# Kernel optimization log

Hardware: AMD Instinct MI355X
Metric: run time of the kernel (lower is better)

Reference implementation:

```python
import math
import jax, jax.numpy as jnp
import numpy as np

B, L, DIM = 8, 8192, 512
H = 8
DH = DIM // H
KS = 13          # kernel_size
DIL = 2          # dilation


def na1d_indices(length, kernel_size, dilation):
    """NATTEN 1D window-start and positional-bias-start indices, vectorized."""
    ns = kernel_size // 2  # neighborhood radius
    i = jnp.arange(length)
    if dilation <= 1:
        ws = jnp.maximum(i - ns, 0) + jnp.where(i + ns >= length, length - i - ns - 1, 0)
        ps = ns + jnp.where(i < ns, ns - i, 0) + jnp.where(i + ns >= length, length - i - 1 - ns, 0)
    else:
        imodd = i % dilation
        a = (length // dilation) * dilation
        b = length - a
        hi = jnp.where(imodd < b,
                       length - b + imodd - 2 * ns * dilation,
                       a + imodd - kernel_size * dilation)
        ni = i - ns * dilation
        at_hi = i + ns * dilation >= length
        ws = jnp.where(ni < 0, imodd, jnp.where(at_hi, hi, ni))
        ps = jnp.where(ni < 0, kernel_size - 1 - i // dilation,
                       jnp.where(at_hi, (length - i - 1) // dilation, ns))
    return ws, ps  # each [L]


def na1d_attention(q, k, v, rpb, kernel_size, dilation):
    """q,k,v: [B,H,L,Dh] (q pre-scaled); rpb: [H, 2*kernel_size-1]."""
    length = q.shape[2]
    ws, ps = na1d_indices(length, kernel_size, dilation)
    # QK + RPB: small fixed loop over kernel taps (K=13), fully vectorized over B,H,L,D
    scores = []
    for j in range(kernel_size):
        idx = ws + j * dilation                      # [L] key index per query
        kj = k[:, :, idx, :]                         # [B,H,L,Dh]
        s = jnp.einsum('bhld,bhld->bhl', q, kj)
        s = s + rpb[:, ps + j][None, :, :]           # [1,H,L]
        scores.append(s)
    attn = jax.nn.softmax(jnp.stack(scores, axis=-1), axis=-1)  # [B,H,L,K]
    # AV
    out = jnp.zeros_like(q)
    for j in range(kernel_size):
        idx = ws + j * dilation
        out = out + attn[..., j:j + 1] * v[:, :, idx, :]
    return out  # [B,H,L,Dh]


def setup_inputs() -> dict:
    key = jax.random.key(0)
    ks = jax.random.split(key, 8)
    s = 1.0 / math.sqrt(DIM)
    return {
        'hidden_states': jax.random.normal(ks[0], (B, L, DIM), dtype=jnp.float32),
        'Wq': jax.random.normal(ks[1], (DIM, DIM), dtype=jnp.float32) * s,
        'bq': jnp.zeros((DIM,), dtype=jnp.float32),
        'Wk': jax.random.normal(ks[2], (DIM, DIM), dtype=jnp.float32) * s,
        'bk': jnp.zeros((DIM,), dtype=jnp.float32),
        'Wv': jax.random.normal(ks[3], (DIM, DIM), dtype=jnp.float32) * s,
        'bv': jnp.zeros((DIM,), dtype=jnp.float32),
        'rpb': jax.random.normal(ks[4], (H, 2 * KS - 1), dtype=jnp.float32) * 0.02,
    }


def reference(hidden_states, Wq, bq, Wk, bk, Wv, bv, rpb):
    def split_heads(x):  # [B,L,DIM] -> [B,H,L,Dh]
        return x.reshape(B, L, H, DH).transpose(0, 2, 1, 3)
    q = split_heads(hidden_states @ Wq + bq) / math.sqrt(DH)
    k = split_heads(hidden_states @ Wk + bk)
    v = split_heads(hidden_states @ Wv + bv)
    ctx = na1d_attention(q, k, v, rpb, KS, DIL)      # [B,H,L,Dh]
    ctx = ctx.transpose(0, 2, 1, 3).reshape(B, L, DIM)
    return ctx
```

## Files before the change

### kernel.cpp

```cpp
#include <hip/hip_runtime.h>
#include <stdint.h>

#define BB   8
#define LL   8192
#define HH   8
#define DH   64
#define DIMM 512
#define KS_  13

typedef unsigned short ushort_t;
typedef __attribute__((ext_vector_type(8))) short bf16x8;
typedef __attribute__((ext_vector_type(4))) float f32x4;

#define AS1 __attribute__((address_space(1)))
#define AS3 __attribute__((address_space(3)))

__device__ __forceinline__ unsigned short f2bf(float f) {
    unsigned u = __float_as_uint(f);
    u += 0x7fffu + ((u >> 16) & 1u);
    return (unsigned short)(u >> 16);
}
__device__ __forceinline__ void unpack8(uint4 u, float* f) {
    f[0] = __uint_as_float(u.x << 16); f[1] = __uint_as_float(u.x & 0xffff0000u);
    f[2] = __uint_as_float(u.y << 16); f[3] = __uint_as_float(u.y & 0xffff0000u);
    f[4] = __uint_as_float(u.z << 16); f[5] = __uint_as_float(u.z & 0xffff0000u);
    f[6] = __uint_as_float(u.w << 16); f[7] = __uint_as_float(u.w & 0xffff0000u);
}
__device__ __forceinline__ uint4 pack8(const float4 a, const float4 b) {
    uint4 u;
    u.x = (unsigned)f2bf(a.x) | ((unsigned)f2bf(a.y) << 16);
    u.y = (unsigned)f2bf(a.z) | ((unsigned)f2bf(a.w) << 16);
    u.z = (unsigned)f2bf(b.x) | ((unsigned)f2bf(b.y) << 16);
    u.w = (unsigned)f2bf(b.z) | ((unsigned)f2bf(b.w) << 16);
    return u;
}

__device__ __forceinline__ void gload16(const void* g, void* l) {
    __builtin_amdgcn_global_load_lds(
        (const AS1 unsigned int*)(unsigned long long)g,
        (AS3 unsigned int*)(unsigned int)(unsigned long long)l,
        16, 0, 0);
}

__global__ void transpose512(const float* __restrict__ Wq,
                             const float* __restrict__ Wk,
                             const float* __restrict__ Wv,
                             ushort_t* __restrict__ Wt) {
    __shared__ float tile[32][33];
    int mtx = blockIdx.z;
    const float* src = (mtx == 0) ? Wq : ((mtx == 1) ? Wk : Wv);
    ushort_t* dst = Wt + (size_t)mtx * 512 * 512;
    int bx = blockIdx.x * 32, by = blockIdx.y * 32;
    int tx = threadIdx.x, ty = threadIdx.y;
    #pragma unroll
    for (int i = 0; i < 32; i += 8)
        tile[ty + i][tx] = src[(size_t)(by + ty + i) * 512 + bx + tx];
    __syncthreads();
    #pragma unroll
    for (int i = 0; i < 32; i += 8)
        dst[(size_t)(bx + ty + i) * 512 + by + tx] = f2bf(tile[tx][ty + i]);
}

__global__ __launch_bounds__(256) void conv_bf16(const float* __restrict__ in,
                                                 ushort_t* __restrict__ out) {
    const size_t n8 = (size_t)BB * LL * DIMM / 8;
    const size_t stride = (size_t)gridDim.x * 256;
    for (size_t i = (size_t)blockIdx.x * 256 + threadIdx.x; i < n8; i += stride) {
        float4 lo = *((const float4*)in + 2 * i);
        float4 hi = *((const float4*)in + 2 * i + 1);
        *((uint4*)out + i) = pack8(lo, hi);
    }
}

__global__ __launch_bounds__(256) void qkv_gemm_lds(
    const ushort_t* __restrict__ Ab,
    const ushort_t* __restrict__ Wt,
    const float* __restrict__ bq,
    const float* __restrict__ bk,
    const float* __restrict__ bv,
    ushort_t* __restrict__ Qo,
    ushort_t* __restrict__ Ko,
    ushort_t* __restrict__ Vo) {
    __shared__ ushort_t sA[128 * 32];
    __shared__ ushort_t sB[128 * 32];

    const int bid = blockIdx.x;
    const int lid = (bid & 7) * 768 + (bid >> 3);
    const int tn  = lid % 12;
    const int tm  = lid / 12;
    const int m0  = tm * 128;
    const int ng  = tn * 128;
    const int mtx = ng >> 9;
    const float* bias = (mtx == 0) ? bq : ((mtx == 1) ? bk : bv);
    ushort_t* Co = (mtx == 0) ? Qo : ((mtx == 1) ? Ko : Vo);
    const float scale = (mtx == 0) ? 0.125f : 1.0f;
    const int n0 = ng & 511;

    const int t    = threadIdx.x;
    const int lane = t & 63;
    const int w    = t >> 6;
    const int wm   = w >> 1, wn = w & 1;
    const int md   = lane & 15, qd = lane >> 4;

    f32x4 acc[4][4];
    const f32x4 zero = {0.f, 0.f, 0.f, 0.f};
    #pragma unroll
    for (int i = 0; i < 4; ++i)
        #pragma unroll
        for (int j = 0; j < 4; ++j) acc[i][j] = zero;

    const int sr = t >> 2;
    const int sc = (t & 3) * 8;
    const ushort_t* ga0 = Ab + (size_t)(m0 + sr) * 512 + sc;
    const ushort_t* ga1 = ga0 + (size_t)64 * 512;
    const ushort_t* gb0 = Wt + (size_t)(ng + sr) * 512 + sc;
    const ushort_t* gb1 = gb0 + (size_t)64 * 512;
    ushort_t* la0 = sA + t * 8;
    ushort_t* la1 = sA + 2048 + t * 8;
    ushort_t* lb0 = sB + t * 8;
    ushort_t* lb1 = sB + 2048 + t * 8;

    const int aoff[4] = { (wm * 64 +  0 + md) * 32 + qd * 8,
                          (wm * 64 + 16 + md) * 32 + qd * 8,
                          (wm * 64 + 32 + md) * 32 + qd * 8,
                          (wm * 64 + 48 + md) * 32 + qd * 8 };
    const int boff[4] = { (wn * 64 +  0 + md) * 32 + qd * 8,
                          (wn * 64 + 16 + md) * 32 + qd * 8,
                          (wn * 64 + 32 + md) * 32 + qd * 8,
                          (wn * 64 + 48 + md) * 32 + qd * 8 };

    for (int kk = 0; kk < 16; ++kk) {
        __syncthreads();
        gload16(ga0 + kk * 32, la0);
        gload16(ga1 + kk * 32, la1);
        gload16(gb0 + kk * 32, lb0);
        gload16(gb1 + kk * 32, lb1);
        __syncthreads();

        bf16x8 af[4], bfv[4];
        #pragma unroll
        for (int mi = 0; mi < 4; ++mi) af[mi]  = *(const bf16x8*)&sA[aoff[mi]];
        #pragma unroll
        for (int ni = 0; ni < 4; ++ni) bfv[ni] = *(const bf16x8*)&sB[boff[ni]];

        #pragma unroll
        for (int mi = 0; mi < 4; ++mi)
            #pragma unroll
            for (int ni = 0; ni < 4; ++ni)
                acc[mi][ni] = __builtin_amdgcn_mfma_f32_16x16x32_bf16(
                    af[mi], bfv[ni], acc[mi][ni], 0, 0, 0);
    }

    #pragma unroll
    for (int ni = 0; ni < 4; ++ni) {
        const int col = n0 + wn * 64 + ni * 16 + md;
        const float bv_ = bias[col];
        #pragma unroll
        for (int mi = 0; mi < 4; ++mi) {
            const int rbase = m0 + wm * 64 + mi * 16 + qd * 4;
            #pragma unroll
            for (int r = 0; r < 4; ++r) {
                float v = (acc[mi][ni][r] + bv_) * scale;
                Co[(size_t)(rbase + r) * 512 + col] = f2bf(v);
            }
        }
    }
}

__global__ __launch_bounds__(256) void qkv_gemm(
    const float* __restrict__ A,
    const ushort_t* __restrict__ Wt,
    const float* __restrict__ bq,
    const float* __restrict__ bk,
    const float* __restrict__ bv,
    ushort_t* __restrict__ Qo,
    ushort_t* __restrict__ Ko,
    ushort_t* __restrict__ Vo) {
    __shared__ ushort_t sA[128 * 32];
    __shared__ ushort_t sB[128 * 32];

    const size_t bofs = (size_t)blockIdx.z * LL * DIMM;
    const int t  = threadIdx.x;
    const int m0 = blockIdx.y * 128;
    const int ng = blockIdx.x * 128;
    const int mtx = ng >> 9;
    const float* bias = (mtx == 0) ? bq : ((mtx == 1) ? bk : bv);
    ushort_t* Co = ((mtx == 0) ? Qo : ((mtx == 1) ? Ko : Vo)) + bofs;
    const float scale = (mtx == 0) ? 0.125f : 1.0f;
    const int n0 = ng & 511;

    const int lane = t & 63;
    const int w    = t >> 6;
    const int wm   = w >> 1, wn = w & 1;
    const int md   = lane & 15, qd = lane >> 4;

    f32x4 acc[4][4];
    const f32x4 zero = {0.f, 0.f, 0.f, 0.f};
    #pragma unroll
    for (int i = 0; i < 4; ++i)
        #pragma unroll
        for (int j = 0; j < 4; ++j) acc[i][j] = zero;

    const int ar = t >> 2;
    const int ac = (t & 3) * 8;
    const float*    gA0 = A + bofs + (size_t)(m0 + ar) * 512 + ac;
    const float*    gA1 = gA0 + (size_t)64 * 512;
    const ushort_t* gB0 = Wt + (size_t)(ng + ar) * 512 + ac;
    const ushort_t* gB1 = gB0 + (size_t)64 * 512;
    ushort_t* lA0 = sA + t * 8;
    ushort_t* lA1 = sA + 2048 + t * 8;
    ushort_t* lB0 = sB + t * 8;
    ushort_t* lB1 = sB + 2048 + t * 8;

    const int aoff[4] = { (wm * 64 +  0 + md) * 32 + qd * 8,
                          (wm * 64 + 16 + md) * 32 + qd * 8,
                          (wm * 64 + 32 + md) * 32 + qd * 8,
                          (wm * 64 + 48 + md) * 32 + qd * 8 };
    const int boff[4] = { (wn * 64 +  0 + md) * 32 + qd * 8,
                          (wn * 64 + 16 + md) * 32 + qd * 8,
                          (wn * 64 + 32 + md) * 32 + qd * 8,
                          (wn * 64 + 48 + md) * 32 + qd * 8 };

    for (int kk = 0; kk < 16; ++kk) {
        float4 a0lo = *(const float4*)(gA0 + kk * 32);
        float4 a0hi = *(const float4*)(gA0 + kk * 32 + 4);
        float4 a1lo = *(const float4*)(gA1 + kk * 32);
        float4 a1hi = *(const float4*)(gA1 + kk * 32 + 4);
        uint4 b0 = *(const uint4*)(gB0 + kk * 32);
        uint4 b1 = *(const uint4*)(gB1 + kk * 32);
        uint4 a0 = pack8(a0lo, a0hi);
        uint4 a1 = pack8(a1lo, a1hi);
        __syncthreads();
        *(uint4*)lA0 = a0;
        *(uint4*)lA1 = a1;
        *(uint4*)lB0 = b0;
        *(uint4*)lB1 = b1;
        __syncthreads();

        bf16x8 af[4], bfv[4];
        #pragma unroll
        for (int mi = 0; mi < 4; ++mi) af[mi]  = *(const bf16x8*)&sA[aoff[mi]];
        #pragma unroll
        for (int ni = 0; ni < 4; ++ni) bfv[ni] = *(const bf16x8*)&sB[boff[ni]];

        #pragma unroll
        for (int mi = 0; mi < 4; ++mi)
            #pragma unroll
            for (int ni = 0; ni < 4; ++ni)
                acc[mi][ni] = __builtin_amdgcn_mfma_f32_16x16x32_bf16(
                    af[mi], bfv[ni], acc[mi][ni], 0, 0, 0);
    }

    #pragma unroll
    for (int ni = 0; ni < 4; ++ni) {
        const int col = n0 + wn * 64 + ni * 16 + md;
        const float bv_ = bias[col];
        #pragma unroll
        for (int mi = 0; mi < 4; ++mi) {
            const int rbase = m0 + wm * 64 + mi * 16 + qd * 4;
            #pragma unroll
            for (int r = 0; r < 4; ++r) {
                float v = (acc[mi][ni][r] + bv_) * scale;
                Co[(size_t)(rbase + r) * 512 + col] = f2bf(v);
            }
        }
    }
}

__global__ __launch_bounds__(256) void na1d_attn(
    const ushort_t* __restrict__ Q,
    const ushort_t* __restrict__ K,
    const ushort_t* __restrict__ V,
    const float* __restrict__ rpb,
    float* __restrict__ O) {
    __shared__ ushort_t sKV[2 * 88 * 72];
    __shared__ float srpb[32];

    const int t  = threadIdx.x;
    const int l0 = blockIdx.x * 64;
    const int h  = blockIdx.y;
    const size_t bofs = (size_t)blockIdx.z * LL * DIMM;

    int p_lo = l0 - 12; if (p_lo < 0) p_lo = 0;
    int p_hi = l0 + 75; if (p_hi > LL - 1) p_hi = LL - 1;
    const int rows = p_hi - p_lo + 1;

    const size_t kvbase = bofs + (size_t)p_lo * DIMM + h * DH;
    const int srow = t >> 3;
    const int scol = (t & 7) * 8;

    ushort_t* sK = sKV;
    ushort_t* sV = sKV + 88 * 72;

    for (int r = srow; r < rows; r += 32)
        *(uint4*)&sK[r * 72 + scol] = *(const uint4*)(K + kvbase + (size_t)r * DIMM + scol);
    for (int r = srow; r < rows; r += 32)
        *(uint4*)&sV[r * 72 + scol] = *(const uint4*)(V + kvbase + (size_t)r * DIMM + scol);
    if (t < 25) srpb[t] = rpb[h * 25 + t];

    const int l    = l0 + (t >> 2);
    const int d0   = (t & 3) * 16;
    const int par  = l & 1;
    const bool lo_e = (l < 12);
    const bool hi_e = (l + 12) >= LL;
    const int ws = lo_e ? par : (hi_e ? (LL - 26 + par) : (l - 12));
    const int ps = lo_e ? (12 - (l >> 1)) : (hi_e ? ((LL - 1 - l) >> 1) : 6);
    const int r0 = ws - p_lo;

    float qf[16];
    {
        const uint4* qg = (const uint4*)(Q + bofs + (size_t)l * DIMM + h * DH + d0);
        #pragma unroll
        for (int c = 0; c < 2; ++c) { uint4 u = qg[c]; unpack8(u, &qf[c * 8]); }
    }
    __syncthreads();

    float s[13];
    #pragma unroll
    for (int j = 0; j < 13; ++j) {
        const uint4* kp = (const uint4*)&sK[(unsigned)(r0 + 2 * j) * 72 + d0];
        float a = 0.f;
        #pragma unroll
        for (int c = 0; c < 2; ++c) {
            uint4 u = kp[c]; float f[8]; unpack8(u, f);
            a += qf[c*8+0]*f[0] + qf[c*8+1]*f[1] + qf[c*8+2]*f[2] + qf[c*8+3]*f[3]
               + qf[c*8+4]*f[4] + qf[c*8+5]*f[5] + qf[c*8+6]*f[6] + qf[c*8+7]*f[7];
        }
        a += __shfl_xor(a, 1);
        a += __shfl_xor(a, 2);
        s[j] = a + srpb[ps + j];
    }

    float mx = s[0];
    #pragma unroll
    for (int j = 1; j < 13; ++j) mx = fmaxf(mx, s[j]);
    float sum = 0.f;
    #pragma unroll
    for (int j = 0; j < 13; ++j) { s[j] = __expf(s[j] - mx); sum += s[j]; }
    const float inv = 1.0f / sum;
    #pragma unroll
    for (int j = 0; j < 13; ++j) s[j] *= inv;

    float of[16];
    #pragma unroll
    for (int d = 0; d < 16; ++d) of[d] = 0.f;
    #pragma unroll
    for (int j = 0; j < 13; ++j) {
        const uint4* vp = (const uint4*)&sV[(unsigned)(r0 + 2 * j) * 72 + d0];
        const float wj = s[j];
        #pragma unroll
        for (int c = 0; c < 2; ++c) {
            uint4 u = vp[c]; float f[8]; unpack8(u, f);
            #pragma unroll
            for (int e = 0; e < 8; ++e) of[c * 8 + e] += wj * f[e];
        }
    }

    __syncthreads();
    float* sO = (float*)sKV;
    {
        float* orow = &sO[(t >> 2) * 66 + d0];
        #pragma unroll
        for (int c = 0; c < 4; ++c) {
            float4 v4; v4.x = of[c*4+0]; v4.y = of[c*4+1];
            v4.z = of[c*4+2]; v4.w = of[c*4+3];
            *(float4*)&orow[c * 4] = v4;
        }
    }
    __syncthreads();
    {
        const int rr = t >> 4;
        const int cc = (t & 15) * 4;
        float* Ob = O + bofs;
        #pragma unroll
        for (int r4 = 0; r4 < 4; ++r4) {
            const int r = rr + r4 * 16;
            *(float4*)(Ob + (size_t)(l0 + r) * DIMM + h * DH + cc) =
                *(const float4*)&sO[r * 66 + cc];
        }
    }
}

extern "C" void kernel_launch(void* const* d_in, const int* in_sizes, int n_in,
                              void* d_out, int out_size, void* d_ws, size_t ws_size,
                              hipStream_t stream) {
    const float* hid = (const float*)d_in[0];
    const float* Wq  = (const float*)d_in[1];
    const float* bq  = (const float*)d_in[2];
    const float* Wk  = (const float*)d_in[3];
    const float* bk  = (const float*)d_in[4];
    const float* Wv  = (const float*)d_in[5];
    const float* bv  = (const float*)d_in[6];
    const float* rpb = (const float*)d_in[7];
    float* out = (float*)d_out;

    ushort_t* ws = (ushort_t*)d_ws;
    ushort_t* Wt = ws;
    const size_t perB = (size_t)LL * DIMM;
    const size_t perF = (size_t)BB * perB;
    const size_t wtEl = (size_t)1536 * 512;
    const size_t need_new = (wtEl + 4 * perF) * sizeof(ushort_t);
    const size_t need_bat = (wtEl + 3 * perF) * sizeof(ushort_t);

    transpose512<<<dim3(16, 16, 3), dim3(32, 8), 0, stream>>>(Wq, Wk, Wv, Wt);

    if (ws_size >= need_new) {
        ushort_t* Ab = Wt + wtEl;
        ushort_t* Qb = Ab + perF;
        ushort_t* Kb = Qb + perF;
        ushort_t* Vb = Kb + perF;
        conv_bf16<<<2048, 256, 0, stream>>>(hid, Ab);
        qkv_gemm_lds<<<dim3(6144), 256, 0, stream>>>(Ab, Wt, bq, bk, bv, Qb, Kb, Vb);
        na1d_attn<<<dim3(LL / 64, HH, BB), 256, 0, stream>>>(Qb, Kb, Vb, rpb, out);
    } else if (ws_size >= need_bat) {
        ushort_t* Qb = Wt + wtEl;
        ushort_t* Kb = Qb + perF;
        ushort_t* Vb = Kb + perF;
        qkv_gemm<<<dim3(12, 64, BB), 256, 0, stream>>>(hid, Wt, bq, bk, bv, Qb, Kb, Vb);
        na1d_attn<<<dim3(LL / 64, HH, BB), 256, 0, stream>>>(Qb, Kb, Vb, rpb, out);
    } else {
        ushort_t* Qb = Wt + wtEl;
        ushort_t* Kb = Qb + perB;
        ushort_t* Vb = Kb + perB;
        for (int b = 0; b < BB; ++b) {
            const float* hb = hid + (size_t)b * perB;
            float*       ob = out + (size_t)b * perB;
            qkv_gemm<<<dim3(12, 64, 1), 256, 0, stream>>>(hb, Wt, bq, bk, bv, Qb, Kb, Vb);
            na1d_attn<<<dim3(LL / 64, HH, 1), 256, 0, stream>>>(Qb, Kb, Vb, rpb, ob);
        }
    }
}
```

Before: 509.3 us.

## Double-buffer QKV GEMM LDS tiles and read K/V directly from global in attention

The QKV GEMM now double-buffers its A and B LDS tiles. It prefetches the next k-slice while the MFMAs run on the current one, which removes one barrier per iteration. The attention kernel drops its cooperative LDS staging of the K/V window and has each thread load its 13 dilated K and V rows straight from global memory, relying on cache for reuse. That avoids the LDS fill and one barrier, at the cost of redundant global/L2 traffic across neighbouring queries.

```diff
diff --git a/kernel.cpp b/kernel.cpp
--- a/kernel.cpp
+++ b/kernel.cpp
@@ -81,8 +81,8 @@
     ushort_t* __restrict__ Qo,
     ushort_t* __restrict__ Ko,
     ushort_t* __restrict__ Vo) {
-    __shared__ ushort_t sA[128 * 32];
-    __shared__ ushort_t sB[128 * 32];
+    __shared__ ushort_t sA[2 * 128 * 32];
+    __shared__ ushort_t sB[2 * 128 * 32];
 
     const int bid = blockIdx.x;
     const int lid = (bid & 7) * 768 + (bid >> 3);
@@ -115,10 +115,8 @@
     const ushort_t* ga1 = ga0 + (size_t)64 * 512;
     const ushort_t* gb0 = Wt + (size_t)(ng + sr) * 512 + sc;
     const ushort_t* gb1 = gb0 + (size_t)64 * 512;
-    ushort_t* la0 = sA + t * 8;
-    ushort_t* la1 = sA + 2048 + t * 8;
-    ushort_t* lb0 = sB + t * 8;
-    ushort_t* lb1 = sB + 2048 + t * 8;
+    const int ld0 = t * 8;
+    const int ld1 = 2048 + t * 8;
 
     const int aoff[4] = { (wm * 64 +  0 + md) * 32 + qd * 8,
                           (wm * 64 + 16 + md) * 32 + qd * 8,
@@ -129,19 +127,27 @@
                           (wn * 64 + 32 + md) * 32 + qd * 8,
                           (wn * 64 + 48 + md) * 32 + qd * 8 };
 
+    gload16(ga0, sA + ld0);
+    gload16(ga1, sA + ld1);
+    gload16(gb0, sB + ld0);
+    gload16(gb1, sB + ld1);
+    __syncthreads();
+
     for (int kk = 0; kk < 16; ++kk) {
-        __syncthreads();
-        gload16(ga0 + kk * 32, la0);
-        gload16(ga1 + kk * 32, la1);
-        gload16(gb0 + kk * 32, lb0);
-        gload16(gb1 + kk * 32, lb1);
-        __syncthreads();
+        const int cur = (kk & 1) << 12;
+        const int nxt = 4096 - cur;
+        if (kk < 15) {
+            gload16(ga0 + (kk + 1) * 32, sA + nxt + ld0);
+            gload16(ga1 + (kk + 1) * 32, sA + nxt + ld1);
+            gload16(gb0 + (kk + 1) * 32, sB + nxt + ld0);
+            gload16(gb1 + (kk + 1) * 32, sB + nxt + ld1);
+        }
 
         bf16x8 af[4], bfv[4];
         #pragma unroll
-        for (int mi = 0; mi < 4; ++mi) af[mi]  = *(const bf16x8*)&sA[aoff[mi]];
-        #pragma unroll
-        for (int ni = 0; ni < 4; ++ni) bfv[ni] = *(const bf16x8*)&sB[boff[ni]];
+        for (int mi = 0; mi < 4; ++mi) af[mi]  = *(const bf16x8*)&sA[cur + aoff[mi]];
+        #pragma unroll
+        for (int ni = 0; ni < 4; ++ni) bfv[ni] = *(const bf16x8*)&sB[cur + boff[ni]];
 
         #pragma unroll
         for (int mi = 0; mi < 4; ++mi)
@@ -149,6 +155,8 @@
             for (int ni = 0; ni < 4; ++ni)
                 acc[mi][ni] = __builtin_amdgcn_mfma_f32_16x16x32_bf16(
                     af[mi], bfv[ni], acc[mi][ni], 0, 0, 0);
+
+        __syncthreads();
     }
 
     #pragma unroll
@@ -273,7 +281,7 @@
     const ushort_t* __restrict__ V,
     const float* __restrict__ rpb,
     float* __restrict__ O) {
-    __shared__ ushort_t sKV[2 * 88 * 72];
+    __shared__ float sO[64 * 66];
     __shared__ float srpb[32];
 
     const int t  = threadIdx.x;
@@ -281,21 +289,6 @@
     const int h  = blockIdx.y;
     const size_t bofs = (size_t)blockIdx.z * LL * DIMM;
 
-    int p_lo = l0 - 12; if (p_lo < 0) p_lo = 0;
-    int p_hi = l0 + 75; if (p_hi > LL - 1) p_hi = LL - 1;
-    const int rows = p_hi - p_lo + 1;
-
-    const size_t kvbase = bofs + (size_t)p_lo * DIMM + h * DH;
-    const int srow = t >> 3;
-    const int scol = (t & 7) * 8;
-
-    ushort_t* sK = sKV;
-    ushort_t* sV = sKV + 88 * 72;
-
-    for (int r = srow; r < rows; r += 32)
-        *(uint4*)&sK[r * 72 + scol] = *(const uint4*)(K + kvbase + (size_t)r * DIMM + scol);
-    for (int r = srow; r < rows; r += 32)
-        *(uint4*)&sV[r * 72 + scol] = *(const uint4*)(V + kvbase + (size_t)r * DIMM + scol);
     if (t < 25) srpb[t] = rpb[h * 25 + t];
 
     const int l    = l0 + (t >> 2);
@@ -305,27 +298,31 @@
     const bool hi_e = (l + 12) >= LL;
     const int ws = lo_e ? par : (hi_e ? (LL - 26 + par) : (l - 12));
     const int ps = lo_e ? (12 - (l >> 1)) : (hi_e ? ((LL - 1 - l) >> 1) : 6);
-    const int r0 = ws - p_lo;
+
+    const ushort_t* kbase = K + bofs + (size_t)ws * DIMM + h * DH + d0;
+    const ushort_t* vbase = V + bofs + (size_t)ws * DIMM + h * DH + d0;
 
     float qf[16];
     {
         const uint4* qg = (const uint4*)(Q + bofs + (size_t)l * DIMM + h * DH + d0);
-        #pragma unroll
-        for (int c = 0; c < 2; ++c) { uint4 u = qg[c]; unpack8(u, &qf[c * 8]); }
+        unpack8(qg[0], qf);
+        unpack8(qg[1], qf + 8);
     }
     __syncthreads();
 
     float s[13];
     #pragma unroll
     for (int j = 0; j < 13; ++j) {
-        const uint4* kp = (const uint4*)&sK[(unsigned)(r0 + 2 * j) * 72 + d0];
+        const uint4* kp = (const uint4*)(kbase + (size_t)(2 * j) * DIMM);
+        uint4 u0 = kp[0], u1 = kp[1];
+        float f[8];
         float a = 0.f;
-        #pragma unroll
-        for (int c = 0; c < 2; ++c) {
-            uint4 u = kp[c]; float f[8]; unpack8(u, f);
-            a += qf[c*8+0]*f[0] + qf[c*8+1]*f[1] + qf[c*8+2]*f[2] + qf[c*8+3]*f[3]
-               + qf[c*8+4]*f[4] + qf[c*8+5]*f[5] + qf[c*8+6]*f[6] + qf[c*8+7]*f[7];
-        }
+        unpack8(u0, f);
+        a += qf[0]*f[0] + qf[1]*f[1] + qf[2]*f[2] + qf[3]*f[3]
+           + qf[4]*f[4] + qf[5]*f[5] + qf[6]*f[6] + qf[7]*f[7];
+        unpack8(u1, f);
+        a += qf[8]*f[0] + qf[9]*f[1] + qf[10]*f[2] + qf[11]*f[3]
+           + qf[12]*f[4] + qf[13]*f[5] + qf[14]*f[6] + qf[15]*f[7];
         a += __shfl_xor(a, 1);
         a += __shfl_xor(a, 2);
         s[j] = a + srpb[ps + j];
@@ -346,18 +343,18 @@
     for (int d = 0; d < 16; ++d) of[d] = 0.f;
     #pragma unroll
     for (int j = 0; j < 13; ++j) {
-        const uint4* vp = (const uint4*)&sV[(unsigned)(r0 + 2 * j) * 72 + d0];
+        const uint4* vp = (const uint4*)(vbase + (size_t)(2 * j) * DIMM);
+        uint4 u0 = vp[0], u1 = vp[1];
         const float wj = s[j];
-        #pragma unroll
-        for (int c = 0; c < 2; ++c) {
-            uint4 u = vp[c]; float f[8]; unpack8(u, f);
-            #pragma unroll
-            for (int e = 0; e < 8; ++e) of[c * 8 + e] += wj * f[e];
-        }
-    }
-
-    __syncthreads();
-    float* sO = (float*)sKV;
+        float f[8];
+        unpack8(u0, f);
+        #pragma unroll
+        for (int e = 0; e < 8; ++e) of[e] += wj * f[e];
+        unpack8(u1, f);
+        #pragma unroll
+        for (int e = 0; e < 8; ++e) of[8 + e] += wj * f[e];
+    }
+
     {
         float* orow = &sO[(t >> 2) * 66 + d0];
         #pragma unroll
```

New measurement: 494.1 us. 1.03x faster.
